# Optimization experiments

Measured on AMD Instinct MI355X. Metric: run time of the kernel, lower is better.

## Reference

```python
import jax, jax.numpy as jnp
import numpy as np

EPS_LOG = 1e-12  # clamp for BCE logs (torch clamps log at -100)


def _gather_feat(feat, ind):
    # feat: [B, C, Hf, Wf] -> gather at flat spatial index ind [B, K] -> [B, K, C]
    B, C, Hf, Wf = feat.shape
    flat = feat.reshape(B, C, Hf * Wf).transpose(0, 2, 1)  # [B, Hf*Wf, C]
    return jnp.take_along_axis(flat, ind[:, :, None], axis=1)  # [B, K, C]


def setup_inputs() -> dict:
    key = jax.random.key(0)
    ks = jax.random.split(key, 6)
    B, K, N, Hf, Wf, H, W = 2, 64, 16, 128, 128, 128, 128
    centers = jax.random.normal(ks[0], (B, 2 * N, Hf, Wf), dtype=jnp.float32)
    radius = jax.random.uniform(ks[1], (B, 1, Hf, Wf), dtype=jnp.float32) * 5.0 + 1.0
    mask = jax.random.uniform(ks[2], (B, K), dtype=jnp.float32)
    ind = jax.random.randint(ks[3], (B, K), 0, Hf * Wf).astype(jnp.int64)
    target = jax.random.uniform(ks[4], (B, K, H, W), dtype=jnp.float32)
    peak = jax.random.uniform(ks[5], (B, K, 2), dtype=jnp.float32) * W
    return {"centers": centers, "radius": radius, "mask": mask, "ind": ind,
            "target": target, "peak": peak}


def reference(centers, radius, mask, ind, target, peak):
    B, C, Hf, Wf = centers.shape
    K = ind.shape[1]
    N = C // 2
    H, W = target.shape[2], target.shape[3]

    pred = _gather_feat(centers, ind)                 # [B, K, 2N]
    pred_radius = _gather_feat(radius, ind)[..., 0]   # [B, K]

    # even channels = x (matched against column index), odd = y (row index)
    pred = pred.reshape(B, K, N, 2) + peak[:, :, None, :]  # [B, K, N, 2]

    # grid[h, w] = (w, h), matching torch's [[ [i, j] for i in range(W)] for j in range(H)]
    gx, gy = jnp.meshgrid(jnp.arange(W, dtype=jnp.float32),
                          jnp.arange(H, dtype=jnp.float32))  # each [H, W]
    grid = jnp.stack([gx, gy], axis=-1)  # [H, W, 2]

    diff = pred[:, :, None, None, :, :] - grid[None, None, :, :, None, :]  # [B,K,H,W,N,2]
    neg_sq = -jnp.sum(diff * diff, axis=-1)                                # [B,K,H,W,N]
    denom = 2.0 * (pred_radius ** 2)[:, :, None, None, None]               # [B,K,1,1,1]
    g = jnp.sum(jnp.exp(neg_sq / denom), axis=-1)                          # [B,K,H,W]
    pred_map = jax.nn.sigmoid(g)  # ceiling == 'sigmoid'

    m = mask[:, :, None, None]  # broadcast over [H, W]
    p = pred_map * m
    t = target * m
    # BCELoss(reduction='mean')
    bce = -(t * jnp.log(jnp.clip(p, EPS_LOG, 1.0)) +
            (1.0 - t) * jnp.log(jnp.clip(1.0 - p, EPS_LOG, 1.0)))
    loss = jnp.mean(bce)
    return (loss, loss)
```

## Files before the change

kernel.cpp:

```cpp
#include <hip/hip_runtime.h>
#include <hip/hip_bf16.h>

#define B_ 2
#define K_ 64
#define N_ 16
#define C_ 32
#define HF_ 128
#define WF_ 128
#define H_ 128
#define W_ 128
#define HW_ (H_ * W_)
#define PIX_PER_THREAD 4
#define PIX_PER_BLOCK (256 * PIX_PER_THREAD)
#define TILES_PER_BK (HW_ / PIX_PER_BLOCK)
#define NBLOCKS (B_ * K_ * TILES_PER_BK)
#define TOTAL_ELEMS ((double)(B_ * K_ * H_ * W_))
#define LOG2E 1.44269504088896f

__global__ __launch_bounds__(256) void gauss_bce_partial(
    const float* __restrict__ centers,
    const float* __restrict__ radius,
    const float* __restrict__ mask,
    const int*   __restrict__ ind,
    const float* __restrict__ target,
    const float* __restrict__ peak,
    float* __restrict__ partials)
{
    __shared__ float sx[N_];
    __shared__ float sy[N_];
    __shared__ float s_c2;
    __shared__ float s_m;
    __shared__ float warp_sums[4];

    const int tid  = threadIdx.x;
    const int bk   = blockIdx.x >> 4;
    const int tile = blockIdx.x & (TILES_PER_BK - 1);
    const int b = bk >> 6;
    const int k = bk & 63;

    if (tid < C_) {
        const int ii = ind[b * K_ + k];
        const float v = centers[(size_t)(b * C_ + tid) * (HF_ * WF_) + ii];
        const int n = tid >> 1;
        if ((tid & 1) == 0) {
            sx[n] = v + peak[(b * K_ + k) * 2 + 0];
        } else {
            sy[n] = v + peak[(b * K_ + k) * 2 + 1];
        }
    } else if (tid == C_) {
        const int ii = ind[b * K_ + k];
        const float r = radius[(size_t)b * (HF_ * WF_) + ii];
        s_c2 = -LOG2E / (2.0f * r * r);
    } else if (tid == C_ + 1) {
        s_m = mask[b * K_ + k];
    }
    __syncthreads();

    const int pix0 = tile * PIX_PER_BLOCK + tid * PIX_PER_THREAD;
    const int h  = pix0 >> 7;
    const int w0 = pix0 & 127;
    const float fy = (float)h;
    const float c2 = s_c2;
    const float m  = s_m;

    const float4 t4 = *(const float4*)&target[((size_t)(b * K_ + k) * H_ + h) * W_ + w0];
    const float tvals[4] = {t4.x, t4.y, t4.z, t4.w};

    float dy2[N_], sxr[N_];
    #pragma unroll
    for (int n = 0; n < N_; ++n) {
        const float dy = sy[n] - fy;
        dy2[n] = dy * dy;
        sxr[n] = sx[n];
    }

    float acc = 0.0f;
    #pragma unroll
    for (int j = 0; j < PIX_PER_THREAD; ++j) {
        const float fx = (float)(w0 + j);
        float g = 0.0f;
        #pragma unroll
        for (int n = 0; n < N_; ++n) {
            const float dx = sxr[n] - fx;
            g += exp2f(__builtin_fmaf(dx, dx, dy2[n]) * c2);
        }
        const float e   = __expf(-g);
        const float sig = __builtin_amdgcn_rcpf(1.0f + e);
        const float p = sig * m;
        const float t = tvals[j] * m;
        const float pc  = fminf(fmaxf(p, 1e-12f), 1.0f);
        const float omp = fminf(fmaxf(1.0f - p, 1e-12f), 1.0f);
        acc += -(t * __logf(pc) + (1.0f - t) * __logf(omp));
    }

    float v = acc;
    #pragma unroll
    for (int off = 32; off > 0; off >>= 1)
        v += __shfl_down(v, off, 64);
    const int lane = tid & 63;
    const int wid  = tid >> 6;
    if (lane == 0) warp_sums[wid] = v;
    __syncthreads();
    if (tid == 0) {
        partials[blockIdx.x] = warp_sums[0] + warp_sums[1] + warp_sums[2] + warp_sums[3];
    }
}

__global__ __launch_bounds__(256) void reduce_final(
    const float* __restrict__ partials, float* __restrict__ out)
{
    __shared__ double warp_sums[4];
    const int tid = threadIdx.x;
    double acc = 0.0;
    #pragma unroll
    for (int i = 0; i < NBLOCKS / 256; ++i)
        acc += (double)partials[i * 256 + tid];

    #pragma unroll
    for (int off = 32; off > 0; off >>= 1)
        acc += __shfl_down(acc, off, 64);
    const int lane = tid & 63;
    const int wid  = tid >> 6;
    if (lane == 0) warp_sums[wid] = acc;
    __syncthreads();
    if (tid == 0) {
        double s = warp_sums[0] + warp_sums[1] + warp_sums[2] + warp_sums[3];
        float loss = (float)(s / TOTAL_ELEMS);
        out[0] = loss;
        out[1] = loss;
    }
}

extern "C" void kernel_launch(void* const* d_in, const int* in_sizes, int n_in,
                              void* d_out, int out_size, void* d_ws, size_t ws_size,
                              hipStream_t stream) {
    const float* centers = (const float*)d_in[0];
    const float* radius  = (const float*)d_in[1];
    const float* mask    = (const float*)d_in[2];
    const int*   ind     = (const int*)d_in[3];
    const float* target  = (const float*)d_in[4];
    const float* peak    = (const float*)d_in[5];
    float* out = (float*)d_out;
    float* partials = (float*)d_ws;

    gauss_bce_partial<<<NBLOCKS, 256, 0, stream>>>(
        centers, radius, mask, ind, target, peak, partials);
    reduce_final<<<1, 256, 0, stream>>>(partials, out);
}
```

Baseline: 84.00 us.

## Factor Gaussian into separable x/y exponentials and simplify BCE log algebra

The kernel now uses the identity exp(-(dx²+dy²)c) = exp(-dx²c)·exp(-dy²c). Each block precomputes per-column x-exponentials (N×W) and per-row y-exponentials into shared memory, then forms the Gaussian sum as a short FMA dot product instead of evaluating N exp2 calls per pixel. The BCE term is rewritten with logs of (1+e) and (1+e−m) plus a precomputed log(mask), which drops the sigmoid reciprocal and the clamps. In exchange it adds shared-memory traffic, an extra barrier, redundant per-block precompute of the x table, and possible underflow or precision differences from the factored products.

```diff
diff --git a/kernel.cpp b/kernel.cpp
--- a/kernel.cpp
+++ b/kernel.cpp
@@ -1,5 +1,4 @@
 #include <hip/hip_runtime.h>
-#include <hip/hip_bf16.h>
 
 #define B_ 2
 #define K_ 64
@@ -12,6 +11,7 @@
 #define HW_ (H_ * W_)
 #define PIX_PER_THREAD 4
 #define PIX_PER_BLOCK (256 * PIX_PER_THREAD)
+#define ROWS_PER_BLOCK (PIX_PER_BLOCK / W_)
 #define TILES_PER_BK (HW_ / PIX_PER_BLOCK)
 #define NBLOCKS (B_ * K_ * TILES_PER_BK)
 #define TOTAL_ELEMS ((double)(B_ * K_ * H_ * W_))
@@ -28,8 +28,11 @@
 {
     __shared__ float sx[N_];
     __shared__ float sy[N_];
+    __shared__ float sEx[N_ * W_];
+    __shared__ float sEy[ROWS_PER_BLOCK][N_];
     __shared__ float s_c2;
     __shared__ float s_m;
+    __shared__ float s_lm;
     __shared__ float warp_sums[4];
 
     const int tid  = threadIdx.x;
@@ -52,45 +55,66 @@
         const float r = radius[(size_t)b * (HF_ * WF_) + ii];
         s_c2 = -LOG2E / (2.0f * r * r);
     } else if (tid == C_ + 1) {
-        s_m = mask[b * K_ + k];
+        const float mm = mask[b * K_ + k];
+        s_m  = mm;
+        s_lm = __logf(fmaxf(mm, 1e-12f));
     }
     __syncthreads();
 
-    const int pix0 = tile * PIX_PER_BLOCK + tid * PIX_PER_THREAD;
-    const int h  = pix0 >> 7;
-    const int w0 = pix0 & 127;
-    const float fy = (float)h;
     const float c2 = s_c2;
+    const int h0 = tile * ROWS_PER_BLOCK;
+
+    #pragma unroll
+    for (int i = 0; i < (N_ * W_) / 256; ++i) {
+        const int idx = tid + i * 256;
+        const float dx = sx[idx >> 7] - (float)(idx & (W_ - 1));
+        sEx[idx] = exp2f(c2 * dx * dx);
+    }
+    if (tid < N_ * ROWS_PER_BLOCK) {
+        const int n = tid & (N_ - 1);
+        const int r = tid >> 4;
+        const float dy = sy[n] - (float)(h0 + r);
+        sEy[r][n] = exp2f(c2 * dy * dy);
+    }
+    __syncthreads();
+
+    const int row = tid >> 5;
+    const int w0  = (tid & 31) << 2;
+    const int h   = h0 + row;
     const float m  = s_m;
+    const float lm = s_lm;
 
     const float4 t4 = *(const float4*)&target[((size_t)(b * K_ + k) * H_ + h) * W_ + w0];
-    const float tvals[4] = {t4.x, t4.y, t4.z, t4.w};
 
-    float dy2[N_], sxr[N_];
+    float ey[N_];
+    #pragma unroll
+    for (int q = 0; q < N_ / 4; ++q) {
+        const float4 e4 = *(const float4*)&sEy[row][q * 4];
+        ey[q * 4 + 0] = e4.x; ey[q * 4 + 1] = e4.y;
+        ey[q * 4 + 2] = e4.z; ey[q * 4 + 3] = e4.w;
+    }
+
+    float gx = 0.0f, gy = 0.0f, gz = 0.0f, gw = 0.0f;
     #pragma unroll
     for (int n = 0; n < N_; ++n) {
-        const float dy = sy[n] - fy;
-        dy2[n] = dy * dy;
-        sxr[n] = sx[n];
+        const float4 x4 = *(const float4*)&sEx[n * W_ + w0];
+        const float e = ey[n];
+        gx = __builtin_fmaf(x4.x, e, gx);
+        gy = __builtin_fmaf(x4.y, e, gy);
+        gz = __builtin_fmaf(x4.z, e, gz);
+        gw = __builtin_fmaf(x4.w, e, gw);
     }
 
+    const float gs[4] = {gx, gy, gz, gw};
+    const float tv[4] = {t4.x, t4.y, t4.z, t4.w};
     float acc = 0.0f;
     #pragma unroll
     for (int j = 0; j < PIX_PER_THREAD; ++j) {
-        const float fx = (float)(w0 + j);
-        float g = 0.0f;
-        #pragma unroll
-        for (int n = 0; n < N_; ++n) {
-            const float dx = sxr[n] - fx;
-            g += exp2f(__builtin_fmaf(dx, dx, dy2[n]) * c2);
-        }
-        const float e   = __expf(-g);
-        const float sig = __builtin_amdgcn_rcpf(1.0f + e);
-        const float p = sig * m;
-        const float t = tvals[j] * m;
-        const float pc  = fminf(fmaxf(p, 1e-12f), 1.0f);
-        const float omp = fminf(fmaxf(1.0f - p, 1e-12f), 1.0f);
-        acc += -(t * __logf(pc) + (1.0f - t) * __logf(omp));
+        const float e  = __expf(-gs[j]);
+        const float L1 = __logf(1.0f + e);
+        const float L2 = __logf(fmaxf(1.0f + e - m, 1e-12f));
+        const float t  = tv[j] * m;
+        acc += (L1 - L2) + t * (L2 - lm);
     }
 
     float v = acc;
```

Result: faster. 75.71 us (-9.9%).
